# Kernel tuning notes

Measured on AMD Instinct MI355X. Metric: run time of the kernel, lower is better.

Reference implementation:

```python
import jax, jax.numpy as jnp
import numpy as np

D = 256       # d_model
HEADS = 8     # n_heads
PTS = 4       # n_points
FF = 1024     # dim_feedforward
HD = D // HEADS
B, Q = 8, 900
HH, WW = 100, 100


def setup_inputs() -> dict:
    key = jax.random.key(0)
    ks = iter(jax.random.split(key, 40))
    p = lambda shape: jax.random.normal(next(ks), shape, dtype=jnp.float32) * 0.02
    inp = {
        "tgt": jax.random.normal(next(ks), (B, Q, D), dtype=jnp.float32),
        "memory": jax.random.normal(next(ks), (B, HH * WW, D), dtype=jnp.float32),
        "H": HH,
        "W": WW,
        # self-attention (nn.MultiheadAttention) params
        "in_proj_w": p((3 * D, D)), "in_proj_b": p((3 * D,)),
        "out_proj_w": p((D, D)), "out_proj_b": p((D,)),
        # layer norms
        "norm1_s": jnp.ones((D,)), "norm1_b": jnp.zeros((D,)),
        "norm2_s": jnp.ones((D,)), "norm2_b": jnp.zeros((D,)),
        "norm3_s": jnp.ones((D,)), "norm3_b": jnp.zeros((D,)),
        # deformable cross-attention params
        "vproj_w": p((D, D)), "vproj_b": p((D,)),
        "offs_w": p((HEADS * PTS * 2, D)), "offs_b": p((HEADS * PTS * 2,)),
        "attw_w": p((HEADS * PTS, D)), "attw_b": p((HEADS * PTS,)),
        "ref_w": p((2, D)), "ref_b": p((2,)),
        "cout_w": p((D, D)), "cout_b": p((D,)),
        # FFN params
        "ffn_w1": p((FF, D)), "ffn_b1": p((FF,)),
        "ffn_w2": p((D, FF)), "ffn_b2": p((D,)),
    }
    return inp


def _layer_norm(x, s, b):
    m = jnp.mean(x, -1, keepdims=True)
    v = jnp.mean((x - m) ** 2, -1, keepdims=True)
    return (x - m) * jax.lax.rsqrt(v + 1e-5) * s + b


def _mha(x, wi, bi, wo, bo):
    b, q, _ = x.shape
    qkv = x @ wi.T + bi
    qh, kh, vh = jnp.split(qkv, 3, axis=-1)
    qh = qh.reshape(b, q, HEADS, HD).transpose(0, 2, 1, 3)
    kh = kh.reshape(b, q, HEADS, HD).transpose(0, 2, 1, 3)
    vh = vh.reshape(b, q, HEADS, HD).transpose(0, 2, 1, 3)
    att = jax.nn.softmax(jnp.einsum('bhqd,bhkd->bhqk', qh, kh) / np.float32(np.sqrt(HD)), axis=-1)
    o = jnp.einsum('bhqk,bhkd->bhqd', att, vh).transpose(0, 2, 1, 3).reshape(b, q, D)
    return o @ wo.T + bo


def _deform_attn(q, mem, H, W, vproj_w, vproj_b, offs_w, offs_b, attw_w, attw_b,
                 ref_w, ref_b, cout_w, cout_b):
    b, nq, _ = q.shape
    # per-query normalized reference points (x, y) in [0,1]
    ref = jax.nn.sigmoid(q @ ref_w.T + ref_b)                         # [B,Q,2]
    offs = (q @ offs_w.T + offs_b).reshape(b, nq, HEADS, PTS, 2)      # [B,Q,h,p,2]
    attw = jax.nn.softmax((q @ attw_w.T + attw_b).reshape(b, nq, HEADS, PTS), axis=-1)
    val = (mem @ vproj_w.T + vproj_b).reshape(b, H * W, HEADS, HD).transpose(0, 2, 1, 3)  # [B,h,HW,hd]
    wh = jnp.array([W, H], dtype=q.dtype)
    loc = ref[:, :, None, None, :] + offs / wh                        # normalized sampling loc
    x = loc[..., 0] * W - 0.5                                         # pixel coords (align_corners=False)
    y = loc[..., 1] * H - 0.5
    x0 = jnp.floor(x); y0 = jnp.floor(y)
    lx = x - x0; ly = y - y0
    x0i = x0.astype(jnp.int32); y0i = y0.astype(jnp.int32)

    def gather(xi, yi):
        valid = ((xi >= 0) & (xi < W) & (yi >= 0) & (yi < H)).astype(q.dtype)
        idx = jnp.clip(yi, 0, H - 1) * W + jnp.clip(xi, 0, W - 1)     # [B,Q,h,p]
        idxt = idx.transpose(0, 2, 1, 3).reshape(b, HEADS, nq * PTS, 1)
        g = jnp.take_along_axis(val, idxt, axis=2)                    # [B,h,Q*p,hd]
        g = g.reshape(b, HEADS, nq, PTS, HD).transpose(0, 2, 1, 3, 4)  # [B,Q,h,p,hd]
        return g * valid[..., None]

    samp = (gather(x0i, y0i) * ((1 - lx) * (1 - ly))[..., None]
            + gather(x0i + 1, y0i) * (lx * (1 - ly))[..., None]
            + gather(x0i, y0i + 1) * ((1 - lx) * ly)[..., None]
            + gather(x0i + 1, y0i + 1) * (lx * ly)[..., None])        # [B,Q,h,p,hd]
    out = jnp.sum(samp * attw[..., None], axis=3).reshape(b, nq, D)
    return out @ cout_w.T + cout_b


def reference(tgt, memory, H, W, in_proj_w, in_proj_b, out_proj_w, out_proj_b,
              norm1_s, norm1_b, norm2_s, norm2_b, norm3_s, norm3_b,
              vproj_w, vproj_b, offs_w, offs_b, attw_w, attw_b, ref_w, ref_b,
              cout_w, cout_b, ffn_w1, ffn_b1, ffn_w2, ffn_b2):
    t2 = _mha(tgt, in_proj_w, in_proj_b, out_proj_w, out_proj_b)
    t = _layer_norm(tgt + t2, norm1_s, norm1_b)
    t2 = _deform_attn(t, memory, H, W, vproj_w, vproj_b, offs_w, offs_b,
                      attw_w, attw_b, ref_w, ref_b, cout_w, cout_b)
    t = _layer_norm(t + t2, norm2_s, norm2_b)
    f = jnp.maximum(t @ ffn_w1.T + ffn_b1, 0) @ ffn_w2.T + ffn_b2
    return _layer_norm(t + f, norm3_s, norm3_b)
```

## Files before the change

kernel.cpp:

```cpp
#include <hip/hip_runtime.h>
#include <hip/hip_bf16.h>

typedef __hip_bfloat16 bf16;
typedef __attribute__((ext_vector_type(8))) short short8;
typedef __attribute__((ext_vector_type(4))) float f32x4;

#define BB 8
#define QQ 900
#define DD 256
#define NH 8
#define HD 32
#define NPTS 4
#define FFD 1024
#define HH 100
#define WW2 100
#define HWTOT 10000

#define QT 64
#define KTC 128
#define NCHUNK ((QQ + KTC - 1) / KTC)
#define QB 4

__device__ inline float tofloat(float x) { return x; }
__device__ inline float tofloat(bf16 x) { return __bfloat162float(x); }
__device__ inline float bf2f(unsigned short u) {
    return __uint_as_float(((unsigned int)u) << 16);
}
__device__ inline void storev(bf16* p, float v) { *p = __float2bfloat16(v); }
__device__ inline void storev(float* p, float v) { *p = v; }

__global__ void pack_kernel(const float* __restrict__ in_proj_w, const float* __restrict__ out_proj_w,
                            const float* __restrict__ cout_w, const float* __restrict__ ffn_w1,
                            const float* __restrict__ ffn_w2, const float* __restrict__ vproj_w,
                            const float* __restrict__ offs_w, const float* __restrict__ attw_w,
                            const float* __restrict__ ref_w, const float* __restrict__ offs_b,
                            const float* __restrict__ attw_b, const float* __restrict__ ref_b,
                            const float* __restrict__ tgt, bf16* __restrict__ wpk,
                            bf16* __restrict__ tgtb, float* __restrict__ dbias) {
    const int idx = blockIdx.x * 256 + threadIdx.x;
    const int TOT = 950272 + 1843200 + 128;
    if (idx >= TOT) return;
    if (idx < 196608) {
        wpk[idx] = __float2bfloat16(in_proj_w[idx]);
    } else if (idx < 262144) {
        wpk[idx] = __float2bfloat16(out_proj_w[idx - 196608]);
    } else if (idx < 327680) {
        wpk[idx] = __float2bfloat16(cout_w[idx - 262144]);
    } else if (idx < 589824) {
        wpk[idx] = __float2bfloat16(ffn_w1[idx - 327680]);
    } else if (idx < 851968) {
        wpk[idx] = __float2bfloat16(ffn_w2[idx - 589824]);
    } else if (idx < 917504) {
        wpk[idx] = __float2bfloat16(vproj_w[idx - 851968]);
    } else if (idx < 950272) {
        const int j = idx - 917504;
        const int r = j >> 8, c = j & 255;
        float v = 0.f;
        if (r < 64) v = offs_w[r * 256 + c];
        else if (r < 96) v = attw_w[(r - 64) * 256 + c];
        else if (r < 98) v = ref_w[(r - 96) * 256 + c];
        wpk[idx] = __float2bfloat16(v);
    } else if (idx < 950272 + 1843200) {
        const int j = idx - 950272;
        tgtb[j] = __float2bfloat16(tgt[j]);
    } else {
        const int j = idx - (950272 + 1843200);
        float v = 0.f;
        if (j < 64) v = offs_b[j];
        else if (j < 96) v = attw_b[j - 64];
        else if (j < 98) v = ref_b[j - 96];
        dbias[j] = v;
    }
}

template <int ACT, typename OT>
__global__ __launch_bounds__(256) void gemm_mfma_kernel(const bf16* __restrict__ A,
                                                        const bf16* __restrict__ W,
                                                        const float* __restrict__ bias,
                                                        OT* __restrict__ C, int M, int N, int K) {
    __shared__ unsigned short As[64][56];
    __shared__ unsigned short Bs[64][56];
    const int bm = blockIdx.y * 64, bn = blockIdx.x * 64;
    const int tid = threadIdx.x;
    const int lane = tid & 63, wave = tid >> 6;
    const int sr = tid >> 2, sc = (tid & 3) * 8;
    f32x4 acc[4] = {{0.f, 0.f, 0.f, 0.f}, {0.f, 0.f, 0.f, 0.f},
                    {0.f, 0.f, 0.f, 0.f}, {0.f, 0.f, 0.f, 0.f}};
    const uint4 zero4 = {0u, 0u, 0u, 0u};
    for (int k0 = 0; k0 < K; k0 += 32) {
        __syncthreads();
        {
            const int arow = bm + sr;
            uint4 a4 = (arow < M) ? *(const uint4*)(A + (size_t)arow * K + k0 + sc) : zero4;
            *(uint4*)&As[sr][sc] = a4;
            const int wrow = bn + sr;
            uint4 b4 = (wrow < N) ? *(const uint4*)(W + (size_t)wrow * K + k0 + sc) : zero4;
            *(uint4*)&Bs[sr][sc] = b4;
        }
        __syncthreads();
        const short8 af = *(const short8*)&As[wave * 16 + (lane & 15)][(lane >> 4) * 8];
#pragma unroll
        for (int ct = 0; ct < 4; ++ct) {
            const short8 bf = *(const short8*)&Bs[ct * 16 + (lane & 15)][(lane >> 4) * 8];
            acc[ct] = __builtin_amdgcn_mfma_f32_16x16x32_bf16(af, bf, acc[ct], 0, 0, 0);
        }
    }
#pragma unroll
    for (int ct = 0; ct < 4; ++ct) {
        const int col = bn + ct * 16 + (lane & 15);
        const float bv = bias[col];
#pragma unroll
        for (int r = 0; r < 4; ++r) {
            const int row = bm + wave * 16 + (lane >> 4) * 4 + r;
            if (row < M) {
                float v = acc[ct][r] + bv;
                if (ACT == 1) v = fmaxf(v, 0.f);
                storev(&C[(size_t)row * N + col], v);
            }
        }
    }
}

__global__ __launch_bounds__(256) void mha_mfma_kernel(const bf16* __restrict__ qkv,
                                                       bf16* __restrict__ o) {
    const int qt = blockIdx.x, h = blockIdx.y, b = blockIdx.z;
    const int tid = threadIdx.x;
    const int lane = tid & 63, wave = tid >> 6;
    const int l15 = lane & 15, g = lane >> 4;
    __shared__ unsigned short Kls[KTC][40];
    __shared__ bf16 Vt[HD][136];
    __shared__ bf16 Pls[4][16][136];
    const size_t base = (size_t)b * QQ * 768;
    const int q0 = qt * QT;

    short8 qa = {0, 0, 0, 0, 0, 0, 0, 0};
    {
        const int qg = q0 + wave * 16 + l15;
        if (qg < QQ)
            qa = *(const short8*)(qkv + base + (size_t)qg * 768 + h * HD + g * 8);
    }
    f32x4 accO[2] = {{0.f, 0.f, 0.f, 0.f}, {0.f, 0.f, 0.f, 0.f}};
    float m_run[4], l_run[4];
#pragma unroll
    for (int r = 0; r < 4; ++r) {
        m_run[r] = -1e30f;
        l_run[r] = 0.f;
    }
    const float scale = 0.17677669529663687f;
    const uint4 zero4 = {0u, 0u, 0u, 0u};

    for (int c = 0; c < NCHUNK; ++c) {
        const int k0 = c * KTC;
        __syncthreads();
        {
            const int part = tid & 3, kr = tid >> 2;
#pragma unroll
            for (int pass = 0; pass < 2; ++pass) {
                const int krr = kr + pass * 64;
                const int kg = k0 + krr;
                uint4 kv = (kg < QQ)
                    ? *(const uint4*)(qkv + base + (size_t)kg * 768 + DD + h * HD + part * 8)
                    : zero4;
                *(uint4*)&Kls[krr][part * 8] = kv;
            }
        }
        {
            const int kr = tid >> 1, ch0 = (tid & 1) * 16;
            const int kg = k0 + kr;
            uint4 v0 = zero4, v1 = zero4;
            if (kg < QQ) {
                const bf16* pv = qkv + base + (size_t)kg * 768 + 2 * DD + h * HD + ch0;
                v0 = *(const uint4*)pv;
                v1 = *(const uint4*)(pv + 8);
            }
            const unsigned short* u0 = (const unsigned short*)&v0;
            const unsigned short* u1 = (const unsigned short*)&v1;
#pragma unroll
            for (int j = 0; j < 8; ++j) {
                ((unsigned short*)&Vt[ch0 + j][kr])[0] = u0[j];
                ((unsigned short*)&Vt[ch0 + 8 + j][kr])[0] = u1[j];
            }
        }
        __syncthreads();

        f32x4 s[8];
#pragma unroll
        for (int t = 0; t < 8; ++t) {
            const short8 kb = *(const short8*)&Kls[t * 16 + l15][g * 8];
            const f32x4 z = {0.f, 0.f, 0.f, 0.f};
            s[t] = __builtin_amdgcn_mfma_f32_16x16x32_bf16(qa, kb, z, 0, 0, 0);
        }
        float mx[4] = {-1e30f, -1e30f, -1e30f, -1e30f};
#pragma unroll
        for (int t = 0; t < 8; ++t) {
            const bool cv = (k0 + t * 16 + l15) < QQ;
#pragma unroll
            for (int r = 0; r < 4; ++r) {
                const float v = cv ? s[t][r] * scale : -1e30f;
                s[t][r] = v;
                mx[r] = fmaxf(mx[r], v);
            }
        }
#pragma unroll
        for (int r = 0; r < 4; ++r) {
            mx[r] = fmaxf(mx[r], __shfl_xor(mx[r], 1));
            mx[r] = fmaxf(mx[r], __shfl_xor(mx[r], 2));
            mx[r] = fmaxf(mx[r], __shfl_xor(mx[r], 4));
            mx[r] = fmaxf(mx[r], __shfl_xor(mx[r], 8));
        }
        float alpha[4], rs[4];
#pragma unroll
        for (int r = 0; r < 4; ++r) {
            const float mn = fmaxf(m_run[r], mx[r]);
            alpha[r] = __expf(m_run[r] - mn);
            m_run[r] = mn;
            rs[r] = 0.f;
        }
#pragma unroll
        for (int t = 0; t < 8; ++t) {
#pragma unroll
            for (int r = 0; r < 4; ++r) {
                const float p = __expf(s[t][r] - m_run[r]);
                rs[r] += p;
                Pls[wave][g * 4 + r][t * 16 + l15] = __float2bfloat16(p);
            }
        }
#pragma unroll
        for (int r = 0; r < 4; ++r) {
            rs[r] += __shfl_xor(rs[r], 1);
            rs[r] += __shfl_xor(rs[r], 2);
            rs[r] += __shfl_xor(rs[r], 4);
            rs[r] += __shfl_xor(rs[r], 8);
            l_run[r] = l_run[r] * alpha[r] + rs[r];
        }
#pragma unroll
        for (int t2 = 0; t2 < 2; ++t2)
#pragma unroll
            for (int r = 0; r < 4; ++r) accO[t2][r] *= alpha[r];
#pragma unroll
        for (int s4 = 0; s4 < 4; ++s4) {
            const short8 pa = *(const short8*)&Pls[wave][l15][s4 * 32 + g * 8];
#pragma unroll
            for (int t2 = 0; t2 < 2; ++t2) {
                const short8 vb = *(const short8*)&Vt[t2 * 16 + l15][s4 * 32 + g * 8];
                accO[t2] = __builtin_amdgcn_mfma_f32_16x16x32_bf16(pa, vb, accO[t2], 0, 0, 0);
            }
        }
    }
#pragma unroll
    for (int r = 0; r < 4; ++r) {
        const int row = q0 + wave * 16 + g * 4 + r;
        if (row < QQ) {
            const float inv = 1.f / l_run[r];
#pragma unroll
            for (int t2 = 0; t2 < 2; ++t2) {
                storev(&o[((size_t)b * QQ + row) * DD + h * HD + t2 * 16 + l15],
                       accO[t2][r] * inv);
            }
        }
    }
}

template <typename TR, typename TO>
__global__ void add_ln_kernel(const TR* __restrict__ resid, const bf16* __restrict__ y,
                              const float* __restrict__ g, const float* __restrict__ bta,
                              TO* __restrict__ out) {
    const int row = blockIdx.x;
    const int tid = threadIdx.x;
    __shared__ float red[256];
    const size_t idx = (size_t)row * DD + tid;
    float v = tofloat(resid[idx]) + tofloat(y[idx]);
    red[tid] = v;
    __syncthreads();
    for (int s = 128; s > 0; s >>= 1) {
        if (tid < s) red[tid] += red[tid + s];
        __syncthreads();
    }
    const float mean = red[0] * (1.f / DD);
    __syncthreads();
    const float d = v - mean;
    red[tid] = d * d;
    __syncthreads();
    for (int s = 128; s > 0; s >>= 1) {
        if (tid < s) red[tid] += red[tid + s];
        __syncthreads();
    }
    const float rstd = rsqrtf(red[0] * (1.f / DD) + 1e-5f);
    storev(&out[idx], d * rstd * g[tid] + bta[tid]);
}

__global__ __launch_bounds__(256) void deform_kernel(
    const float* __restrict__ dots, const float* __restrict__ mem,
    const bf16* __restrict__ vwpk, const float* __restrict__ vproj_b,
    bf16* __restrict__ samp) {
    const int qt = blockIdx.x, b = blockIdx.y;
    const int tid = threadIdx.x;
    const int q0 = qt * QB;
    __shared__ int sidx[QB][32][4];
    __shared__ float swt[QB][32][4];
    __shared__ float wsum[QB][NH];
    __shared__ float G[QB * NH * DD];

    if (tid < 128) {
        const int q = tid >> 5, hp = tid & 31;
        const float* dr = dots + ((size_t)b * QQ + q0 + q) * 128;
        const float ox = dr[hp * 2], oy = dr[hp * 2 + 1];
        float ad = dr[64 + hp];
        const float rx = dr[96], ry = dr[97];
        float mx = ad;
        mx = fmaxf(mx, __shfl_xor(mx, 1));
        mx = fmaxf(mx, __shfl_xor(mx, 2));
        float e = __expf(ad - mx);
        float sm = e;
        sm += __shfl_xor(sm, 1);
        sm += __shfl_xor(sm, 2);
        const float a = e / sm;
        const float refx = 1.f / (1.f + __expf(-rx));
        const float refy = 1.f / (1.f + __expf(-ry));
        const float x = (refx + ox * (1.f / WW2)) * WW2 - 0.5f;
        const float y = (refy + oy * (1.f / HH)) * HH - 0.5f;
        const float x0f = floorf(x), y0f = floorf(y);
        const float lx = x - x0f, ly = y - y0f;
        const int x0 = (int)x0f, y0 = (int)y0f;
        const float cw[4] = {(1 - lx) * (1 - ly), lx * (1 - ly), (1 - lx) * ly, lx * ly};
        const int cx[4] = {x0, x0 + 1, x0, x0 + 1};
        const int cy[4] = {y0, y0, y0 + 1, y0 + 1};
        float cs = 0.f;
#pragma unroll
        for (int cc = 0; cc < 4; ++cc) {
            const bool valid = cx[cc] >= 0 && cx[cc] < WW2 && cy[cc] >= 0 && cy[cc] < HH;
            const int xi = min(max(cx[cc], 0), WW2 - 1);
            const int yi = min(max(cy[cc], 0), HH - 1);
            sidx[q][hp][cc] = yi * WW2 + xi;
            const float w = valid ? a * cw[cc] : 0.f;
            swt[q][hp][cc] = w;
            cs += w;
        }
        cs += __shfl_xor(cs, 1);
        cs += __shfl_xor(cs, 2);
        if ((hp & 3) == 0) wsum[q][hp >> 2] = cs;
    }
    __syncthreads();

    {
        const int q = tid >> 6, c4o = (tid & 63) * 4;
        const float* mb = mem + (size_t)b * HWTOT * DD;
        float4* Gp = (float4*)G;
#pragma unroll
        for (int h = 0; h < NH; ++h) {
            float4 acc = {0.f, 0.f, 0.f, 0.f};
#pragma unroll
            for (int p = 0; p < NPTS; ++p) {
                const int hp = h * NPTS + p;
#pragma unroll
                for (int cc = 0; cc < 4; ++cc) {
                    const float w = swt[q][hp][cc];
                    const float4 v = *(const float4*)(mb + (size_t)sidx[q][hp][cc] * DD + c4o);
                    acc.x += w * v.x;
                    acc.y += w * v.y;
                    acc.z += w * v.z;
                    acc.w += w * v.w;
                }
            }
            Gp[(q * NH + h) * 64 + (tid & 63)] = acc;
        }
    }
    __syncthreads();

    {
        const int ch = tid, h = ch >> 5;
        const bf16* wr = vwpk + (size_t)ch * DD;
        const float bv = vproj_b[ch];
        float acc[QB];
#pragma unroll
        for (int q = 0; q < QB; ++q) acc[q] = wsum[q][h] * bv;
        for (int k = 0; k < DD; k += 8) {
            const uint4 u = *(const uint4*)(wr + k);
            const unsigned short* us = (const unsigned short*)&u;
            float wf[8];
#pragma unroll
            for (int j = 0; j < 8; ++j) wf[j] = bf2f(us[j]);
#pragma unroll
            for (int q = 0; q < QB; ++q) {
                const float* gq = &G[(q * NH + h) * DD + k];
#pragma unroll
                for (int j = 0; j < 8; ++j) acc[q] += gq[j] * wf[j];
            }
        }
#pragma unroll
        for (int q = 0; q < QB; ++q) {
            storev(&samp[((size_t)b * QQ + q0 + q) * DD + ch], acc[q]);
        }
    }
}

extern "C" void kernel_launch(void* const* d_in, const int* in_sizes, int n_in,
                              void* d_out, int out_size, void* d_ws, size_t ws_size,
                              hipStream_t stream) {
    const float* tgt = (const float*)d_in[0];
    const float* memory = (const float*)d_in[1];
    const float* in_proj_w = (const float*)d_in[4];
    const float* in_proj_b = (const float*)d_in[5];
    const float* out_proj_w = (const float*)d_in[6];
    const float* out_proj_b = (const float*)d_in[7];
    const float* norm1_s = (const float*)d_in[8];
    const float* norm1_b = (const float*)d_in[9];
    const float* norm2_s = (const float*)d_in[10];
    const float* norm2_b = (const float*)d_in[11];
    const float* norm3_s = (const float*)d_in[12];
    const float* norm3_b = (const float*)d_in[13];
    const float* vproj_w = (const float*)d_in[14];
    const float* vproj_b = (const float*)d_in[15];
    const float* offs_w = (const float*)d_in[16];
    const float* offs_b = (const float*)d_in[17];
    const float* attw_w = (const float*)d_in[18];
    const float* attw_b = (const float*)d_in[19];
    const float* ref_w = (const float*)d_in[20];
    const float* ref_b = (const float*)d_in[21];
    const float* cout_w = (const float*)d_in[22];
    const float* cout_b = (const float*)d_in[23];
    const float* ffn_w1 = (const float*)d_in[24];
    const float* ffn_b1 = (const float*)d_in[25];
    const float* ffn_w2 = (const float*)d_in[26];
    const float* ffn_b2 = (const float*)d_in[27];

    const int M = BB * QQ;
    bf16* ws = (bf16*)d_ws;
    size_t off = 0;
    bf16* qkv = ws + off;  off += (size_t)M * 768;
    bf16* o = ws + off;    off += (size_t)M * DD;
    bf16* t1 = ws + off;   off += (size_t)M * DD;
    bf16* tmp = ws + off;  off += (size_t)M * DD;
    bf16* ffh = ws + off;  off += (size_t)M * FFD;
    bf16* tgtb = ws + off; off += (size_t)M * DD;
    bf16* wpk = ws + off;  off += 950272;
    float* dbias = (float*)(ws + off);
    bf16* samp = o;
    bf16* t2n = qkv;
    float* dots = (float*)ffh;

    bf16* w_in = wpk;
    bf16* w_out = wpk + 196608;
    bf16* w_cout = wpk + 262144;
    bf16* w_ffn1 = wpk + 327680;
    bf16* w_ffn2 = wpk + 589824;
    bf16* w_vproj = wpk + 851968;
    bf16* w_dots = wpk + 917504;

    const int MT = (M + 63) / 64;

    pack_kernel<<<(950272 + 1843200 + 128 + 255) / 256, 256, 0, stream>>>(
        in_proj_w, out_proj_w, cout_w, ffn_w1, ffn_w2, vproj_w, offs_w, attw_w, ref_w,
        offs_b, attw_b, ref_b, tgt, wpk, tgtb, dbias);
    gemm_mfma_kernel<0, bf16><<<dim3(12, MT), 256, 0, stream>>>(tgtb, w_in, in_proj_b, qkv,
                                                                M, 768, DD);
    mha_mfma_kernel<<<dim3((QQ + QT - 1) / QT, NH, BB), 256, 0, stream>>>(qkv, o);
    gemm_mfma_kernel<0, bf16><<<dim3(4, MT), 256, 0, stream>>>(o, w_out, out_proj_b, tmp,
                                                               M, DD, DD);
    add_ln_kernel<float, bf16><<<M, 256, 0, stream>>>(tgt, tmp, norm1_s, norm1_b, t1);
    gemm_mfma_kernel<0, float><<<dim3(2, MT), 256, 0, stream>>>(t1, w_dots, dbias, dots,
                                                                M, 128, DD);
    deform_kernel<<<dim3(QQ / QB, BB), 256, 0, stream>>>(dots, memory, w_vproj, vproj_b, samp);
    gemm_mfma_kernel<0, bf16><<<dim3(4, MT), 256, 0, stream>>>(samp, w_cout, cout_b, tmp,
                                                               M, DD, DD);
    add_ln_kernel<bf16, bf16><<<M, 256, 0, stream>>>(t1, tmp, norm2_s, norm2_b, t2n);
    gemm_mfma_kernel<1, bf16><<<dim3(16, MT), 256, 0, stream>>>(t2n, w_ffn1, ffn_b1, ffh,
                                                                M, FFD, DD);
    gemm_mfma_kernel<0, bf16><<<dim3(4, MT), 256, 0, stream>>>(ffh, w_ffn2, ffn_b2, tmp,
                                                               M, DD, FFD);
    add_ln_kernel<bf16, float><<<M, 256, 0, stream>>>(t2n, tmp, norm3_s, norm3_b,
                                                      (float*)d_out);
}
```

Before: 382.9 us.

## Split deformable attention into gather kernel and per-head MFMA value-projection GEMM

The fused deformable kernel, which gathered bilinear samples into shared memory and then ran the per-head value projection with scalar FMAs, is split in two. A gather kernel writes per-head sampled memory features in bf16 to workspace along with per-head weight sums. A new MFMA GEMM kernel then applies the head-blocked value projection and folds in the bias scaled by the weight sum. This moves the projection onto matrix cores and frees shared memory in the gather kernel. The cost is a large intermediate buffer (M*8*256 bf16) written and read through global memory, an extra launch, and added bf16 rounding.

```diff
diff --git a/kernel.cpp b/kernel.cpp
--- a/kernel.cpp
+++ b/kernel.cpp
@@ -289,17 +289,14 @@
     storev(&out[idx], d * rstd * g[tid] + bta[tid]);
 }
 
-__global__ __launch_bounds__(256) void deform_kernel(
+__global__ __launch_bounds__(256) void deform_gather_kernel(
     const float* __restrict__ dots, const float* __restrict__ mem,
-    const bf16* __restrict__ vwpk, const float* __restrict__ vproj_b,
-    bf16* __restrict__ samp) {
+    bf16* __restrict__ G, float* __restrict__ wsumg) {
     const int qt = blockIdx.x, b = blockIdx.y;
     const int tid = threadIdx.x;
     const int q0 = qt * QB;
     __shared__ int sidx[QB][32][4];
     __shared__ float swt[QB][32][4];
-    __shared__ float wsum[QB][NH];
-    __shared__ float G[QB * NH * DD];
 
     if (tid < 128) {
         const int q = tid >> 5, hp = tid & 31;
@@ -338,58 +335,83 @@
         }
         cs += __shfl_xor(cs, 1);
         cs += __shfl_xor(cs, 2);
-        if ((hp & 3) == 0) wsum[q][hp >> 2] = cs;
+        if ((hp & 3) == 0) wsumg[((size_t)b * QQ + q0 + q) * NH + (hp >> 2)] = cs;
     }
     __syncthreads();
 
     {
-        const int q = tid >> 6, c4o = (tid & 63) * 4;
+        const int q = tid >> 6, cbase = (tid & 63) * 4;
         const float* mb = mem + (size_t)b * HWTOT * DD;
-        float4* Gp = (float4*)G;
+        bf16* gq = G + ((size_t)(b * QQ + q0 + q) * NH) * DD + cbase;
 #pragma unroll
         for (int h = 0; h < NH; ++h) {
             float4 acc = {0.f, 0.f, 0.f, 0.f};
 #pragma unroll
             for (int p = 0; p < NPTS; ++p) {
                 const int hp = h * NPTS + p;
-#pragma unroll
-                for (int cc = 0; cc < 4; ++cc) {
-                    const float w = swt[q][hp][cc];
-                    const float4 v = *(const float4*)(mb + (size_t)sidx[q][hp][cc] * DD + c4o);
-                    acc.x += w * v.x;
-                    acc.y += w * v.y;
-                    acc.z += w * v.z;
-                    acc.w += w * v.w;
-                }
-            }
-            Gp[(q * NH + h) * 64 + (tid & 63)] = acc;
-        }
-    }
-    __syncthreads();
-
-    {
-        const int ch = tid, h = ch >> 5;
-        const bf16* wr = vwpk + (size_t)ch * DD;
-        const float bv = vproj_b[ch];
-        float acc[QB];
-#pragma unroll
-        for (int q = 0; q < QB; ++q) acc[q] = wsum[q][h] * bv;
-        for (int k = 0; k < DD; k += 8) {
-            const uint4 u = *(const uint4*)(wr + k);
-            const unsigned short* us = (const unsigned short*)&u;
-            float wf[8];
-#pragma unroll
-            for (int j = 0; j < 8; ++j) wf[j] = bf2f(us[j]);
-#pragma unroll
-            for (int q = 0; q < QB; ++q) {
-                const float* gq = &G[(q * NH + h) * DD + k];
-#pragma unroll
-                for (int j = 0; j < 8; ++j) acc[q] += gq[j] * wf[j];
-            }
-        }
-#pragma unroll
-        for (int q = 0; q < QB; ++q) {
-            storev(&samp[((size_t)b * QQ + q0 + q) * DD + ch], acc[q]);
+                const int4 ix = *(const int4*)sidx[q][hp];
+                const float4 wt = *(const float4*)swt[q][hp];
+                const float4 v0 = *(const float4*)(mb + (size_t)ix.x * DD + cbase);
+                const float4 v1 = *(const float4*)(mb + (size_t)ix.y * DD + cbase);
+                const float4 v2 = *(const float4*)(mb + (size_t)ix.z * DD + cbase);
+                const float4 v3 = *(const float4*)(mb + (size_t)ix.w * DD + cbase);
+                acc.x += wt.x * v0.x + wt.y * v1.x + wt.z * v2.x + wt.w * v3.x;
+                acc.y += wt.x * v0.y + wt.y * v1.y + wt.z * v2.y + wt.w * v3.y;
+                acc.z += wt.x * v0.z + wt.y * v1.z + wt.z * v2.z + wt.w * v3.z;
+                acc.w += wt.x * v0.w + wt.y * v1.w + wt.z * v2.w + wt.w * v3.w;
+            }
+            bf16 out4[4] = {__float2bfloat16(acc.x), __float2bfloat16(acc.y),
+                            __float2bfloat16(acc.z), __float2bfloat16(acc.w)};
+            *(uint2*)(gq + (size_t)h * DD) = *(const uint2*)out4;
+        }
+    }
+}
+
+__global__ __launch_bounds__(256) void gemm_vproj_kernel(
+    const bf16* __restrict__ G, const bf16* __restrict__ Wv,
+    const float* __restrict__ vb, const float* __restrict__ wsumg,
+    bf16* __restrict__ samp, int M) {
+    __shared__ unsigned short As[64][40];
+    __shared__ unsigned short Bs[32][40];
+    const int h = blockIdx.x, bm = blockIdx.y * 64;
+    const int tid = threadIdx.x;
+    const int lane = tid & 63, wave = tid >> 6;
+    const int l15 = lane & 15, g = lane >> 4;
+    const int sr = tid >> 2, sc = (tid & 3) * 8;
+    f32x4 acc[2] = {{0.f, 0.f, 0.f, 0.f}, {0.f, 0.f, 0.f, 0.f}};
+    const uint4 zero4 = {0u, 0u, 0u, 0u};
+    for (int k0 = 0; k0 < DD; k0 += 32) {
+        __syncthreads();
+        {
+            const int arow = bm + sr;
+            uint4 a4 = (arow < M)
+                ? *(const uint4*)(G + ((size_t)arow * NH + h) * DD + k0 + sc)
+                : zero4;
+            *(uint4*)&As[sr][sc] = a4;
+            if (sr < 32) {
+                uint4 b4 = *(const uint4*)(Wv + (size_t)(h * 32 + sr) * DD + k0 + sc);
+                *(uint4*)&Bs[sr][sc] = b4;
+            }
+        }
+        __syncthreads();
+        const short8 af = *(const short8*)&As[wave * 16 + l15][g * 8];
+#pragma unroll
+        for (int ct = 0; ct < 2; ++ct) {
+            const short8 bf = *(const short8*)&Bs[ct * 16 + l15][g * 8];
+            acc[ct] = __builtin_amdgcn_mfma_f32_16x16x32_bf16(af, bf, acc[ct], 0, 0, 0);
+        }
+    }
+#pragma unroll
+    for (int ct = 0; ct < 2; ++ct) {
+        const int col = h * 32 + ct * 16 + l15;
+        const float bv = vb[col];
+#pragma unroll
+        for (int r = 0; r < 4; ++r) {
+            const int row = bm + wave * 16 + g * 4 + r;
+            if (row < M) {
+                const float v = acc[ct][r] + bv * wsumg[(size_t)row * NH + h];
+                storev(&samp[(size_t)row * DD + col], v);
+            }
         }
     }
 }
@@ -434,7 +456,9 @@
     bf16* ffh = ws + off;  off += (size_t)M * FFD;
     bf16* tgtb = ws + off; off += (size_t)M * DD;
     bf16* wpk = ws + off;  off += 950272;
-    float* dbias = (float*)(ws + off);
+    float* dbias = (float*)(ws + off); off += 256;
+    float* wsumg = (float*)(ws + off); off += (size_t)M * NH * 2;
+    bf16* Gws = ws + off;  off += (size_t)M * NH * DD;
     bf16* samp = o;
     bf16* t2n = qkv;
     float* dots = (float*)ffh;
@@ -460,7 +484,9 @@
     add_ln_kernel<float, bf16><<<M, 256, 0, stream>>>(tgt, tmp, norm1_s, norm1_b, t1);
     gemm_mfma_kernel<0, float><<<dim3(2, MT), 256, 0, stream>>>(t1, w_dots, dbias, dots,
                                                                 M, 128, DD);
-    deform_kernel<<<dim3(QQ / QB, BB), 256, 0, stream>>>(dots, memory, w_vproj, vproj_b, samp);
+    deform_gather_kernel<<<dim3(QQ / QB, BB), 256, 0, stream>>>(dots, memory, Gws, wsumg);
+    gemm_vproj_kernel<<<dim3(NH, MT), 256, 0, stream>>>(Gws, w_vproj, vproj_b, wsumg,
+                                                        samp, M);
     gemm_mfma_kernel<0, bf16><<<dim3(4, MT), 256, 0, stream>>>(samp, w_cout, cout_b, tmp,
                                                                M, DD, DD);
     add_ln_kernel<bf16, bf16><<<M, 256, 0, stream>>>(t1, tmp, norm2_s, norm2_b, t2n);
```

Measured after the change: 369.3 us. 1.04x faster.
